# Optimization experiments

Hardware: AMD Instinct MI355X
Metric: run time of the kernel (lower is better)

Reference implementation:

```python
import jax, jax.numpy as jnp
import numpy as np

EPS_D = 2e-6      # epsilon in derivative_function
BN_EPS = 1e-5     # nn.BatchNorm1d default eps


def _derivative_1d(y, x, n_C, n_T):
    # ---- context window: nearest neighbor among the first n_C points ----
    cx = x[:, :n_C]                      # [B, nC, 1]
    cy = y[:, :n_C]                      # [B, nC, 1]
    # pairwise L2 distances [B, nC, nC]
    dist = jnp.linalg.norm(cx[:, :, None, :] - cx[:, None, :, :], axis=-1)
    ix = jnp.argsort(dist, axis=-1)[:, :, 1]          # nearest non-self neighbor
    x_cl = jnp.take_along_axis(cx, ix[..., None], axis=1)
    y_cl = jnp.take_along_axis(cy, ix[..., None], axis=1)
    x_rep = cx - x_cl
    y_rep = cy - y_cl
    deriv = y_rep / (EPS_D + jnp.linalg.norm(x_rep, axis=-1, keepdims=True))

    # ---- target window: NN among causally-allowed pool of n_C+n_T points ----
    tx = x[:, n_C:n_C + n_T]             # [B, nT, 1]
    ty = y[:, n_C:n_C + n_T]
    px = x[:, :n_C + n_T]                # [B, nC+nT, 1]
    py = y[:, :n_C + n_T]
    dist_t = jnp.linalg.norm(tx[:, :, None, :] - px[:, None, :, :], axis=-1)  # [B,nT,nC+nT]
    mask = ~jnp.tril(jnp.ones((n_T, n_C + n_T), dtype=bool), k=n_C)           # forbid future points
    dist_t = dist_t + mask.astype(dist_t.dtype) * 1000.0
    ixt = jnp.argsort(dist_t, axis=-1)[:, :, 1]
    x_clt = jnp.take_along_axis(px, ixt[..., None], axis=1)
    y_clt = jnp.take_along_axis(py, ixt[..., None], axis=1)
    x_rep_t = tx - x_clt
    y_rep_t = ty - y_clt
    deriv_t = y_rep_t / (EPS_D + jnp.linalg.norm(x_rep_t, axis=-1, keepdims=True))

    y_diff = jnp.concatenate([y_rep, y_rep_t], axis=1)
    x_diff = jnp.concatenate([x_rep, x_rep_t], axis=1)
    d = jnp.concatenate([deriv, deriv_t], axis=1)
    x_n = jnp.concatenate([x_cl, x_clt], axis=1)
    y_n = jnp.concatenate([y_cl, y_clt], axis=1)
    return y_diff, x_diff, d, x_n, y_n


def reference(y, x, bn_weight, bn_bias, n_C, n_T):
    y_diff, x_diff, d, x_n, y_n = _derivative_1d(y, x, n_C, n_T)
    d_1 = jnp.where(jnp.isnan(d), jnp.asarray(10000.0, d.dtype), d)
    d_2 = jnp.where(jnp.abs(d) > 200.0, jnp.asarray(0.0, d.dtype), d)
    # BatchNorm1d(1) in training mode over the flattened [-1, 1] view: batch stats
    flat = d_2.reshape(-1)
    mean = flat.mean()
    var = flat.var()  # biased variance, matching torch training normalization
    d_norm = ((flat - mean) / jnp.sqrt(var + BN_EPS) * bn_weight[0] + bn_bias[0]).reshape(d_2.shape)
    d_label = (d_2 == d_1).astype(d.dtype)
    d_out = jnp.concatenate([d_norm, d_label], axis=-1)
    return (y_diff, x_diff, d_out, x_n, y_n)


def setup_inputs() -> dict:
    key = jax.random.key(0)
    k1, k2 = jax.random.split(key)
    B, N = 8, 2048
    n_C, n_T = 1024, 1024
    y = jax.random.normal(k1, (B, N, 1), dtype=jnp.float32)
    x = jax.random.normal(k2, (B, N, 1), dtype=jnp.float32)
    bn_weight = jnp.ones((1,), dtype=jnp.float32)
    bn_bias = jnp.zeros((1,), dtype=jnp.float32)
    return {"y": y, "x": x, "bn_weight": bn_weight, "bn_bias": bn_bias, "n_C": n_C, "n_T": n_T}
```

## Files before the change

kernel.cpp:

```cpp
#include <hip/hip_runtime.h>

#define BB   8
#define NN   2048
#define NC   1024
#define TOT  (BB * NN)
#define NBLK 4096

#define OFF_YDIFF 0
#define OFF_XDIFF (TOT)
#define OFF_DOUT  (2 * TOT)
#define OFF_XN    (4 * TOT)
#define OFF_YN    (5 * TOT)

__device__ __forceinline__ void lex_merge(float& d1, int& i1, float& d2, int& i2,
                                          float od1, int oi1, float od2, int oi2)
{
    const bool  lt1 = (od1 < d1) || (od1 == d1 && oi1 < i1);
    const float w1  = lt1 ? od1 : d1;   const int wi1 = lt1 ? oi1 : i1;
    const float l1  = lt1 ? d1  : od1;  const int li1 = lt1 ? i1  : oi1;
    const float w2  = lt1 ? od2 : d2;   const int wi2 = lt1 ? oi2 : i2;
    const bool  lt2 = (l1 < w2) || (l1 == w2 && li1 < wi2);
    d1 = w1; i1 = wi1;
    d2 = lt2 ? l1 : w2;  i2 = lt2 ? li1 : wi2;
}

#define UPD(a, p) {                                          \
    if      ((a) < b1) { b2 = b1; j2 = j1; b1 = (a); j1 = (p); } \
    else if ((a) < b2) { b2 = (a); j2 = (p); } }

__global__ __launch_bounds__(256) void DE_89404039234069_nn(
    const float* __restrict__ y, const float* __restrict__ x,
    float* __restrict__ out, double* __restrict__ psum, double* __restrict__ psq)
{
    __shared__ float xs[NN];
    __shared__ float ys[NN];
    __shared__ float d2sh[4];

    const int tid  = threadIdx.x;
    const int blk  = blockIdx.x;
    const int b    = blk >> 9;
    const int base = b * NN;
    const int i0   = (blk & 511) * 4;

    {
        const float4* xg = (const float4*)(x + base);
        const float4* yg = (const float4*)(y + base);
        float4* xs4 = (float4*)xs;
        float4* ys4 = (float4*)ys;
        xs4[tid]       = xg[tid];
        xs4[tid + 256] = xg[tid + 256];
        ys4[tid]       = yg[tid];
        ys4[tid + 256] = yg[tid + 256];
    }
    __syncthreads();

    const int wave = tid >> 6, lane = tid & 63;
    const int i    = i0 + wave;
    const float xi = xs[i];
    const int limit = (i < NC) ? NC : (i + 1);
    const int kfull = limit >> 8;

    float b1 = 1e30f, b2 = 1e30f;
    int   j1 = 0,     j2 = 0;

    for (int k = 0; k < kfull; ++k) {
        const int p0 = k * 256 + lane * 4;
        const float4 v = *(const float4*)&xs[p0];
        const float a0 = fabsf(v.x - xi);
        const float a1 = fabsf(v.y - xi);
        const float a2 = fabsf(v.z - xi);
        const float a3 = fabsf(v.w - xi);
        UPD(a0, p0); UPD(a1, p0 + 1); UPD(a2, p0 + 2); UPD(a3, p0 + 3);
    }
    if (kfull * 256 < limit) {
        const int p0 = kfull * 256 + lane * 4;
        const float4 v = *(const float4*)&xs[p0];
        float a0 = fabsf(v.x - xi);
        float a1 = fabsf(v.y - xi);
        float a2 = fabsf(v.z - xi);
        float a3 = fabsf(v.w - xi);
        if (p0     >= limit) a0 = 1e30f;
        if (p0 + 1 >= limit) a1 = 1e30f;
        if (p0 + 2 >= limit) a2 = 1e30f;
        if (p0 + 3 >= limit) a3 = 1e30f;
        UPD(a0, p0); UPD(a1, p0 + 1); UPD(a2, p0 + 2); UPD(a3, p0 + 3);
    }

    for (int off = 1; off < 64; off <<= 1) {
        const float od1 = __shfl_xor(b1, off, 64);
        const int   oi1 = __shfl_xor(j1, off, 64);
        const float od2 = __shfl_xor(b2, off, 64);
        const int   oi2 = __shfl_xor(j2, off, 64);
        lex_merge(b1, j1, b2, j2, od1, oi1, od2, oi2);
    }

    if (lane == 0) {
        const int   j    = j2;
        const float xj   = xs[j];
        const float yj   = ys[j];
        const float yi   = ys[i];
        const float xrep = xi - xj;
        const float yrep = yi - yj;
        const float d    = yrep / (2e-6f + fabsf(xrep));

        const float d1v   = (d != d) ? 10000.0f : d;
        const float d2v   = (fabsf(d) > 200.0f) ? 0.0f : d;
        const float label = (d2v == d1v) ? 1.0f : 0.0f;

        const int gi = base + i;
        out[OFF_YDIFF + gi]        = yrep;
        out[OFF_XDIFF + gi]        = xrep;
        out[OFF_XN + gi]           = xj;
        out[OFF_YN + gi]           = yj;
        out[OFF_DOUT + 2 * gi]     = d2v;
        out[OFF_DOUT + 2 * gi + 1] = label;
        d2sh[wave] = d2v;
    }
    __syncthreads();
    if (tid == 0) {
        double s = 0.0, q = 0.0;
        #pragma unroll
        for (int w = 0; w < 4; ++w) {
            const double v = (double)d2sh[w];
            s += v; q += v * v;
        }
        psum[blk] = s;
        psq[blk]  = q;
    }
}

__global__ __launch_bounds__(256) void DE_89404039234069_bn(
    float* __restrict__ out, const double* __restrict__ psum,
    const double* __restrict__ psq,
    const float* __restrict__ bw, const float* __restrict__ bb)
{
    __shared__ double ws[4], wq[4];
    __shared__ float mean_s, scale_s;

    const int tid = threadIdx.x;
    double s = 0.0, q = 0.0;
    for (int k = tid; k < NBLK; k += 256) { s += psum[k]; q += psq[k]; }
    #pragma unroll
    for (int off = 32; off > 0; off >>= 1) {
        s += __shfl_down(s, off, 64);
        q += __shfl_down(q, off, 64);
    }
    const int lane = tid & 63, wave = tid >> 6;
    if (lane == 0) { ws[wave] = s; wq[wave] = q; }
    __syncthreads();
    if (tid == 0) {
        const double S = ws[0] + ws[1] + ws[2] + ws[3];
        const double Q = wq[0] + wq[1] + wq[2] + wq[3];
        const double mean = S * (1.0 / (double)TOT);
        const double var  = Q * (1.0 / (double)TOT) - mean * mean;
        mean_s  = (float)mean;
        scale_s = (float)(1.0 / sqrt(var + 1e-5));
    }
    __syncthreads();

    const float w    = bw[0];
    const float bias = bb[0];
    const int   idx  = blockIdx.x * 256 + tid;
    const float v    = out[OFF_DOUT + 2 * idx];
    out[OFF_DOUT + 2 * idx] = (v - mean_s) * scale_s * w + bias;
}

extern "C" void kernel_launch(void* const* d_in, const int* in_sizes, int n_in,
                              void* d_out, int out_size, void* d_ws, size_t ws_size,
                              hipStream_t stream)
{
    const float* y  = (const float*)d_in[0];
    const float* x  = (const float*)d_in[1];
    const float* bw = (const float*)d_in[2];
    const float* bb = (const float*)d_in[3];
    float*  out  = (float*)d_out;
    double* psum = (double*)d_ws;
    double* psq  = psum + NBLK;

    DE_89404039234069_nn<<<NBLK, 256, 0, stream>>>(y, x, out, psum, psq);
    DE_89404039234069_bn<<<64, 256, 0, stream>>>(out, psum, psq, bw, bb);
}
```

Baseline: 79.83 us.

## Process eight query points per wave to reuse shared-memory candidate loads

Each wave now handles eight query points at once instead of one, so each float4 read of candidate x values from shared memory is reused across eight distance/top-2 updates. The grid shrinks eightfold, the top-2 update becomes branchless via fmin/fmax and selects, and lane-local indices are encoded compactly and expanded before the cross-lane merge. The y array is no longer staged in shared memory; y values are read from global memory in the epilogue, and outputs are written as float4 vectors with per-wave partial sums. Costs are higher register pressure and an eightfold shuffle reduction per wave, and the epilogue is serialized on lane 0.

```diff
diff --git a/kernel.cpp b/kernel.cpp
--- a/kernel.cpp
+++ b/kernel.cpp
@@ -4,7 +4,9 @@
 #define NN   2048
 #define NC   1024
 #define TOT  (BB * NN)
-#define NBLK 4096
+#define PW   8
+#define NWAVE (TOT / PW)
+#define NBLK  (NWAVE / 4)
 
 #define OFF_YDIFF 0
 #define OFF_XDIFF (TOT)
@@ -24,108 +26,150 @@
     d2 = lt2 ? l1 : w2;  i2 = lt2 ? li1 : wi2;
 }
 
-#define UPD(a, p) {                                          \
-    if      ((a) < b1) { b2 = b1; j2 = j1; b1 = (a); j1 = (p); } \
-    else if ((a) < b2) { b2 = (a); j2 = (p); } }
+#define UPDK(k, a, enc) {                                         \
+    const bool lt1 = (a) < b1[k];                                 \
+    const bool lt2 = (a) < b2[k];                                 \
+    j2[k] = lt1 ? j1[k] : (lt2 ? (enc) : j2[k]);                  \
+    j1[k] = lt1 ? (enc) : j1[k];                                  \
+    b2[k] = fminf(b2[k], fmaxf(b1[k], (a)));                      \
+    b1[k] = fminf(b1[k], (a)); }
 
 __global__ __launch_bounds__(256) void DE_89404039234069_nn(
     const float* __restrict__ y, const float* __restrict__ x,
     float* __restrict__ out, double* __restrict__ psum, double* __restrict__ psq)
 {
     __shared__ float xs[NN];
-    __shared__ float ys[NN];
-    __shared__ float d2sh[4];
 
     const int tid  = threadIdx.x;
     const int blk  = blockIdx.x;
-    const int b    = blk >> 9;
+    const int b    = blk >> 6;
     const int base = b * NN;
-    const int i0   = (blk & 511) * 4;
-
-    {
-        const float4* xg = (const float4*)(x + base);
-        const float4* yg = (const float4*)(y + base);
-        float4* xs4 = (float4*)xs;
-        float4* ys4 = (float4*)ys;
-        xs4[tid]       = xg[tid];
-        xs4[tid + 256] = xg[tid + 256];
-        ys4[tid]       = yg[tid];
-        ys4[tid + 256] = yg[tid + 256];
-    }
+
+    const float4* xg  = (const float4*)(x + base);
+    float4*       xs4 = (float4*)xs;
+    xs4[tid]       = xg[tid];
+    xs4[tid + 256] = xg[tid + 256];
     __syncthreads();
 
     const int wave = tid >> 6, lane = tid & 63;
-    const int i    = i0 + wave;
-    const float xi = xs[i];
-    const int limit = (i < NC) ? NC : (i + 1);
-    const int kfull = limit >> 8;
-
-    float b1 = 1e30f, b2 = 1e30f;
-    int   j1 = 0,     j2 = 0;
-
-    for (int k = 0; k < kfull; ++k) {
-        const int p0 = k * 256 + lane * 4;
-        const float4 v = *(const float4*)&xs[p0];
-        const float a0 = fabsf(v.x - xi);
-        const float a1 = fabsf(v.y - xi);
-        const float a2 = fabsf(v.z - xi);
-        const float a3 = fabsf(v.w - xi);
-        UPD(a0, p0); UPD(a1, p0 + 1); UPD(a2, p0 + 2); UPD(a3, p0 + 3);
-    }
-    if (kfull * 256 < limit) {
-        const int p0 = kfull * 256 + lane * 4;
-        const float4 v = *(const float4*)&xs[p0];
-        float a0 = fabsf(v.x - xi);
-        float a1 = fabsf(v.y - xi);
-        float a2 = fabsf(v.z - xi);
-        float a3 = fabsf(v.w - xi);
-        if (p0     >= limit) a0 = 1e30f;
-        if (p0 + 1 >= limit) a1 = 1e30f;
-        if (p0 + 2 >= limit) a2 = 1e30f;
-        if (p0 + 3 >= limit) a3 = 1e30f;
-        UPD(a0, p0); UPD(a1, p0 + 1); UPD(a2, p0 + 2); UPD(a3, p0 + 3);
-    }
-
+    const int i0   = (blk & 63) * 32 + wave * 8;
+
+    float xi[PW], b1[PW], b2[PW];
+    int   j1[PW], j2[PW];
+    #pragma unroll
+    for (int k = 0; k < PW; ++k) {
+        xi[k] = xs[i0 + k];
+        b1[k] = 1e30f; b2[k] = 1e30f; j1[k] = 0; j2[k] = 0;
+    }
+
+    if (i0 < NC) {
+        #pragma unroll
+        for (int s = 0; s < 4; ++s) {
+            const float4 v = xs4[(s << 6) + lane];
+            #pragma unroll
+            for (int k = 0; k < PW; ++k) {
+                UPDK(k, fabsf(v.x - xi[k]), 4 * s + 0);
+                UPDK(k, fabsf(v.y - xi[k]), 4 * s + 1);
+                UPDK(k, fabsf(v.z - xi[k]), 4 * s + 2);
+                UPDK(k, fabsf(v.w - xi[k]), 4 * s + 3);
+            }
+        }
+    } else {
+        const int F      = (i0 + 1) >> 8;
+        const int maxlim = i0 + 8;
+        int s = 0;
+        for (; s < F; ++s) {
+            const float4 v = xs4[(s << 6) + lane];
+            const int e0 = 4 * s;
+            #pragma unroll
+            for (int k = 0; k < PW; ++k) {
+                UPDK(k, fabsf(v.x - xi[k]), e0 + 0);
+                UPDK(k, fabsf(v.y - xi[k]), e0 + 1);
+                UPDK(k, fabsf(v.z - xi[k]), e0 + 2);
+                UPDK(k, fabsf(v.w - xi[k]), e0 + 3);
+            }
+        }
+        for (; (s << 8) < maxlim; ++s) {
+            const float4 v  = xs4[(s << 6) + lane];
+            const int    p0 = (s << 8) + (lane << 2);
+            const int    e0 = 4 * s;
+            #pragma unroll
+            for (int k = 0; k < PW; ++k) {
+                const int lim = i0 + k + 1;
+                const float a0 = (p0     < lim) ? fabsf(v.x - xi[k]) : 1e30f;
+                const float a1 = (p0 + 1 < lim) ? fabsf(v.y - xi[k]) : 1e30f;
+                const float a2 = (p0 + 2 < lim) ? fabsf(v.z - xi[k]) : 1e30f;
+                const float a3 = (p0 + 3 < lim) ? fabsf(v.w - xi[k]) : 1e30f;
+                UPDK(k, a0, e0 + 0);
+                UPDK(k, a1, e0 + 1);
+                UPDK(k, a2, e0 + 2);
+                UPDK(k, a3, e0 + 3);
+            }
+        }
+    }
+
+    float D1[PW], D2[PW];
+    int   J1[PW], J2[PW];
+    #pragma unroll
+    for (int k = 0; k < PW; ++k) {
+        D1[k] = b1[k]; D2[k] = b2[k];
+        J1[k] = ((j1[k] >> 2) << 8) | (lane << 2) | (j1[k] & 3);
+        J2[k] = ((j2[k] >> 2) << 8) | (lane << 2) | (j2[k] & 3);
+    }
     for (int off = 1; off < 64; off <<= 1) {
-        const float od1 = __shfl_xor(b1, off, 64);
-        const int   oi1 = __shfl_xor(j1, off, 64);
-        const float od2 = __shfl_xor(b2, off, 64);
-        const int   oi2 = __shfl_xor(j2, off, 64);
-        lex_merge(b1, j1, b2, j2, od1, oi1, od2, oi2);
+        #pragma unroll
+        for (int k = 0; k < PW; ++k) {
+            const float od1 = __shfl_xor(D1[k], off, 64);
+            const int   oi1 = __shfl_xor(J1[k], off, 64);
+            const float od2 = __shfl_xor(D2[k], off, 64);
+            const int   oi2 = __shfl_xor(J2[k], off, 64);
+            lex_merge(D1[k], J1[k], D2[k], J2[k], od1, oi1, od2, oi2);
+        }
     }
 
     if (lane == 0) {
-        const int   j    = j2;
-        const float xj   = xs[j];
-        const float yj   = ys[j];
-        const float yi   = ys[i];
-        const float xrep = xi - xj;
-        const float yrep = yi - yj;
-        const float d    = yrep / (2e-6f + fabsf(xrep));
-
-        const float d1v   = (d != d) ? 10000.0f : d;
-        const float d2v   = (fabsf(d) > 200.0f) ? 0.0f : d;
-        const float label = (d2v == d1v) ? 1.0f : 0.0f;
-
-        const int gi = base + i;
-        out[OFF_YDIFF + gi]        = yrep;
-        out[OFF_XDIFF + gi]        = xrep;
-        out[OFF_XN + gi]           = xj;
-        out[OFF_YN + gi]           = yj;
-        out[OFF_DOUT + 2 * gi]     = d2v;
-        out[OFF_DOUT + 2 * gi + 1] = label;
-        d2sh[wave] = d2v;
-    }
-    __syncthreads();
-    if (tid == 0) {
+        const float4 yi4a = ((const float4*)(y + base + i0))[0];
+        const float4 yi4b = ((const float4*)(y + base + i0))[1];
+        const float yiv[PW] = { yi4a.x, yi4a.y, yi4a.z, yi4a.w,
+                                yi4b.x, yi4b.y, yi4b.z, yi4b.w };
+        float yd[PW], xd[PW], dn[PW], lb[PW], xnv[PW], ynv[PW];
         double s = 0.0, q = 0.0;
         #pragma unroll
-        for (int w = 0; w < 4; ++w) {
-            const double v = (double)d2sh[w];
-            s += v; q += v * v;
-        }
-        psum[blk] = s;
-        psq[blk]  = q;
+        for (int k = 0; k < PW; ++k) {
+            const int   j    = J2[k];
+            const float xj   = xs[j];
+            const float yj   = y[base + j];
+            const float xrep = xi[k] - xj;
+            const float yrep = yiv[k] - yj;
+            const float d    = yrep / (2e-6f + fabsf(xrep));
+            const float d1v  = (d != d) ? 10000.0f : d;
+            const float d2v  = (fabsf(d) > 200.0f) ? 0.0f : d;
+            yd[k]  = yrep; xd[k] = xrep; xnv[k] = xj; ynv[k] = yj;
+            dn[k]  = d2v;
+            lb[k]  = (d2v == d1v) ? 1.0f : 0.0f;
+            s += (double)d2v; q += (double)d2v * (double)d2v;
+        }
+        const int gi = base + i0;
+        float4* oyd = (float4*)(out + OFF_YDIFF + gi);
+        float4* oxd = (float4*)(out + OFF_XDIFF + gi);
+        float4* oxn = (float4*)(out + OFF_XN + gi);
+        float4* oyn = (float4*)(out + OFF_YN + gi);
+        float4* odo = (float4*)(out + OFF_DOUT + 2 * gi);
+        oyd[0] = make_float4(yd[0], yd[1], yd[2], yd[3]);
+        oyd[1] = make_float4(yd[4], yd[5], yd[6], yd[7]);
+        oxd[0] = make_float4(xd[0], xd[1], xd[2], xd[3]);
+        oxd[1] = make_float4(xd[4], xd[5], xd[6], xd[7]);
+        oxn[0] = make_float4(xnv[0], xnv[1], xnv[2], xnv[3]);
+        oxn[1] = make_float4(xnv[4], xnv[5], xnv[6], xnv[7]);
+        oyn[0] = make_float4(ynv[0], ynv[1], ynv[2], ynv[3]);
+        oyn[1] = make_float4(ynv[4], ynv[5], ynv[6], ynv[7]);
+        odo[0] = make_float4(dn[0], lb[0], dn[1], lb[1]);
+        odo[1] = make_float4(dn[2], lb[2], dn[3], lb[3]);
+        odo[2] = make_float4(dn[4], lb[4], dn[5], lb[5]);
+        odo[3] = make_float4(dn[6], lb[6], dn[7], lb[7]);
+        const int gw = blk * 4 + wave;
+        psum[gw] = s;
+        psq[gw]  = q;
     }
 }
 
@@ -139,7 +183,7 @@
 
     const int tid = threadIdx.x;
     double s = 0.0, q = 0.0;
-    for (int k = tid; k < NBLK; k += 256) { s += psum[k]; q += psq[k]; }
+    for (int k = tid; k < NWAVE; k += 256) { s += psum[k]; q += psq[k]; }
     #pragma unroll
     for (int off = 32; off > 0; off >>= 1) {
         s += __shfl_down(s, off, 64);
@@ -175,7 +219,7 @@
     const float* bb = (const float*)d_in[3];
     float*  out  = (float*)d_out;
     double* psum = (double*)d_ws;
-    double* psq  = psum + NBLK;
+    double* psq  = psum + NWAVE;
 
     DE_89404039234069_nn<<<NBLK, 256, 0, stream>>>(y, x, out, psum, psq);
     DE_89404039234069_bn<<<64, 256, 0, stream>>>(out, psum, psq, bw, bb);
```

Measured after the change: 85.14 us. +6.7%, slower.
